# Optimization experiments

Measured on AMD Instinct MI355X. Metric: run time of the kernel, lower is better.

The kernel has to match this reference:

```python
import jax, jax.numpy as jnp
import numpy as np

NUM_HEADS = 16


def rotary_pos_emb(x):
    # x: [b, h, s, d] with interleaved rotary pairs (d even)
    d, s = x.shape[-1], x.shape[-2]
    ts = jnp.arange(0, d, 2, dtype=jnp.float32)
    inv_freqs = 10000.0 ** (-ts / d)                      # [d/2]
    grid = jnp.arange(s, dtype=jnp.float32)[:, None] * inv_freqs[None, :]  # [s, d/2]
    sin = jnp.repeat(jnp.sin(grid), 2, axis=-1)           # [s, d]
    cos = jnp.repeat(jnp.cos(grid), 2, axis=-1)           # [s, d]
    x1, x2 = x[..., ::2], x[..., 1::2]
    xs = jnp.stack([-x2, x1], axis=-1).reshape(x.shape)   # rotate pairs
    return x * cos + xs * sin


def setup_inputs() -> dict:
    key = jax.random.key(0)
    ks = jax.random.split(key, 6)
    b, l, d = 2, 2048, 1024
    x = jax.random.normal(ks[0], (b, l, d), dtype=jnp.float32)
    # additive causal mask: 0 on/below diag, large negative above
    causal = jnp.tril(jnp.ones((l, l), dtype=bool))
    mask = jnp.where(causal, 0.0, -1e9).astype(jnp.float32)[None, None]  # [1,1,l,l]
    s = 0.01  # VarianceScaling(0.01)-ish small init
    Wq = jax.random.normal(ks[1], (d, d), dtype=jnp.float32) * s
    Wk = jax.random.normal(ks[2], (d, d), dtype=jnp.float32) * s
    Wv = jax.random.normal(ks[3], (d, d), dtype=jnp.float32) * s
    Wo = jax.random.normal(ks[4], (d, d), dtype=jnp.float32) * s
    return {"x": x, "mask": mask, "Wq": Wq, "Wk": Wk, "Wv": Wv, "Wo": Wo}


def reference(x, mask, Wq, Wk, Wv, Wo):
    b, l, d = x.shape
    h = NUM_HEADS
    k_sz = d // h
    split = lambda t: t.reshape(b, l, h, k_sz).transpose(0, 2, 1, 3)  # b h l k
    # NOTE: original scales q by 1/sqrt(model_dim) (not key_size), before RoPE
    q = split(x @ Wq / jnp.sqrt(jnp.float32(d)))
    q = rotary_pos_emb(q)
    k = rotary_pos_emb(split(x @ Wk))
    v = split(x @ Wv)
    logits = jnp.einsum('bhik,bhjk->bhij', q, k) + mask   # [b,h,l,l]
    a = jax.nn.softmax(logits, axis=-1)
    y = jnp.einsum('bhij,bhjv->bhiv', a, v)               # [b,h,l,k]
    y = y.transpose(0, 2, 1, 3).reshape(b, l, d)
    return y @ Wo
```

## Files before the change

kernel.cpp:

```cpp
#include <hip/hip_runtime.h>
#include <math.h>

#define L 2048
#define D 1024
#define H 16
#define KS 64
#define BBATCH 2

typedef float f32x4 __attribute__((ext_vector_type(4)));
typedef short s16x8 __attribute__((ext_vector_type(8)));

__device__ __forceinline__ ushort f2bf(float f) {
    union { float f; unsigned u; } v; v.f = f;
    unsigned lsb = (v.u >> 16) & 1u;
    v.u += 0x7fffu + lsb;
    return (ushort)(v.u >> 16);
}

__device__ __forceinline__ unsigned fbits(float f) {
    union { float f; unsigned u; } v; v.f = f; return v.u;
}

__device__ __forceinline__ void gl_lds16(const ushort* g, ushort* l) {
    __builtin_amdgcn_global_load_lds(
        (const __attribute__((address_space(1))) unsigned int*)g,
        (__attribute__((address_space(3))) unsigned int*)l, 16, 0, 0);
}

__global__ __launch_bounds__(256)
void prep(const float* __restrict__ x,
          const float* __restrict__ W0, const float* __restrict__ W1,
          const float* __restrict__ W2, const float* __restrict__ W3,
          ushort* __restrict__ xb, ushort* __restrict__ Wt,
          float2* __restrict__ tab)
{
    __shared__ float T[32][33];
    const int bid = blockIdx.x;
    const int tid = threadIdx.x;
    if (bid < 4096) {
        const int i = bid * 1024 + tid * 4;
        const float4 v = *(const float4*)&x[i];
        ushort4 p = make_ushort4(f2bf(v.x), f2bf(v.y), f2bf(v.z), f2bf(v.w));
        *(ushort4*)&xb[i] = p;
    } else if (bid < 8192) {
        const int t = bid - 4096;
        const int z = t >> 10;
        const float* W = (z == 0) ? W0 : (z == 1) ? W1 : (z == 2) ? W2 : W3;
        ushort* out = Wt + (size_t)z * D * D;
        const int r0 = ((t >> 5) & 31) * 32, c0 = (t & 31) * 32;
        const int tr = tid >> 3, tc = (tid & 7) * 4;
        const float4 v = *(const float4*)&W[(size_t)(r0 + tr) * D + c0 + tc];
        T[tr][tc + 0] = v.x; T[tr][tc + 1] = v.y;
        T[tr][tc + 2] = v.z; T[tr][tc + 3] = v.w;
        __syncthreads();
        ushort4 p = make_ushort4(f2bf(T[tc + 0][tr]), f2bf(T[tc + 1][tr]),
                                 f2bf(T[tc + 2][tr]), f2bf(T[tc + 3][tr]));
        *(ushort4*)&out[(size_t)(c0 + tr) * D + r0 + tc] = p;
    } else {
        const int idx = (bid - 8192) * 256 + tid;
        const int dd2 = idx >> 11, s = idx & 2047;
        const float inv = __expf(-(float)(2 * dd2) * (9.210340371976184f / 64.0f));
        float sn, cs;
        sincosf((float)s * inv, &sn, &cs);
        tab[idx] = make_float2(cs, sn);
    }
}

__global__ __launch_bounds__(256)
void qkv_gemm(const ushort* __restrict__ A, const ushort* __restrict__ B,
              const float2* __restrict__ tab,
              ushort* __restrict__ Qo, ushort* __restrict__ Ko,
              ushort* __restrict__ Vto)
{
    __shared__ __align__(16) ushort smem[18432];
    ushort* As = smem;
    ushort* Bs = smem + 4096;

    const int tid  = threadIdx.x;
    const int wv   = tid >> 6, lane = tid & 63;
    const int i16  = lane & 15, quad = lane >> 4;
    const int wr   = wv >> 1, wc = wv & 1;
    const int m0   = blockIdx.y * 128;
    const int n0   = blockIdx.x * 128;

    f32x4 acc[4][4];
    #pragma unroll
    for (int i = 0; i < 4; ++i)
        #pragma unroll
        for (int j = 0; j < 4; ++j) acc[i][j] = (f32x4){0.f, 0.f, 0.f, 0.f};

    for (int k0 = 0; k0 < D; k0 += 32) {
        __syncthreads();
        {
            int c = wv * 64 + lane;
            gl_lds16(A + (size_t)(m0 + (c >> 2)) * D + k0 + (c & 3) * 8,
                     As + (size_t)(wv * 64) * 8);
            c = 256 + wv * 64 + lane;
            gl_lds16(A + (size_t)(m0 + (c >> 2)) * D + k0 + (c & 3) * 8,
                     As + (size_t)(256 + wv * 64) * 8);
        }
        {
            int c = wv * 64 + lane;
            gl_lds16(B + (size_t)(n0 + (c >> 2)) * D + k0 + (c & 3) * 8,
                     Bs + (size_t)(wv * 64) * 8);
            c = 256 + wv * 64 + lane;
            gl_lds16(B + (size_t)(n0 + (c >> 2)) * D + k0 + (c & 3) * 8,
                     Bs + (size_t)(256 + wv * 64) * 8);
        }
        __syncthreads();
        s16x8 af[4], bf[4];
        #pragma unroll
        for (int mt = 0; mt < 4; ++mt)
            af[mt] = *(const s16x8*)&As[(wr * 64 + mt * 16 + i16) * 32 + quad * 8];
        #pragma unroll
        for (int nt = 0; nt < 4; ++nt)
            bf[nt] = *(const s16x8*)&Bs[(wc * 64 + nt * 16 + i16) * 32 + quad * 8];
        #pragma unroll
        for (int mt = 0; mt < 4; ++mt)
            #pragma unroll
            for (int nt = 0; nt < 4; ++nt)
                acc[mt][nt] = __builtin_amdgcn_mfma_f32_16x16x32_bf16(
                    af[mt], bf[nt], acc[mt][nt], 0, 0, 0);
    }

    if (m0 < 2048) {
        const bool isQ = (m0 < 1024);
        ushort* out = isQ ? Qo : Ko;
        const int mb = isQ ? m0 : (m0 - 1024);
        #pragma unroll
        for (int mt = 0; mt < 4; ++mt)
            #pragma unroll
            for (int nt = 0; nt < 4; ++nt) {
                const int token = n0 + wc * 64 + nt * 16 + i16;
                const int b = token >> 11, s = token & 2047;
                const int dim = mb + wr * 64 + mt * 16 + quad * 4;
                const int hh = dim >> 6, dd = dim & 63;
                ushort4 p;
                #pragma unroll
                for (int pr = 0; pr < 2; ++pr) {
                    float e = acc[mt][nt][2 * pr];
                    float o = acc[mt][nt][2 * pr + 1];
                    if (isQ) { e *= 0.03125f; o *= 0.03125f; }
                    const float2 cssn = tab[(size_t)((dd >> 1) + pr) * 2048 + s];
                    const float ne = e * cssn.x - o * cssn.y;
                    const float no = o * cssn.x + e * cssn.y;
                    if (pr == 0) { p.x = f2bf(ne); p.y = f2bf(no); }
                    else         { p.z = f2bf(ne); p.w = f2bf(no); }
                }
                *(ushort4*)&out[((size_t)(b * H + hh) * L + s) * KS + dd] = p;
            }
    } else {
        __syncthreads();
        ushort* T = smem + wv * 4608;
        const int vbase = (m0 - 2048) + wr * 64;
        const int tbase = n0 + wc * 64;
        #pragma unroll
        for (int mt = 0; mt < 4; ++mt)
            #pragma unroll
            for (int nt = 0; nt < 4; ++nt) {
                const int tl = nt * 16 + i16;
                #pragma unroll
                for (int r = 0; r < 4; ++r)
                    T[(mt * 16 + quad * 4 + r) * 72 + tl] = f2bf(acc[mt][nt][r]);
            }
        __builtin_amdgcn_s_waitcnt(0);
        const int tl0 = (lane & 7) * 8;
        #pragma unroll
        for (int c = 0; c < 8; ++c) {
            const int vl = c * 8 + (lane >> 3);
            const s16x8 val = *(const s16x8*)&T[vl * 72 + tl0];
            const int vdim = vbase + vl;
            const int hh = vdim >> 6, dd = vdim & 63;
            const int token0 = tbase + tl0;
            const int b = token0 >> 11, s0 = token0 & 2047;
            *(s16x8*)&Vto[((size_t)(b * H + hh) * KS + dd) * L + s0] = val;
        }
    }
}

__global__ __launch_bounds__(256)
void oproj_gemm(const ushort* __restrict__ A, const ushort* __restrict__ B,
                float* __restrict__ out)
{
    __shared__ __align__(16) ushort As[128 * 32];
    __shared__ __align__(16) ushort Bs[64 * 32];
    const int tid  = threadIdx.x;
    const int wv   = tid >> 6, lane = tid & 63;
    const int i16  = lane & 15, quad = lane >> 4;
    const int wr   = wv >> 1, wc = wv & 1;
    const int m0   = blockIdx.y * 128;
    const int n0   = blockIdx.x * 64;

    f32x4 acc[4][2];
    #pragma unroll
    for (int i = 0; i < 4; ++i)
        #pragma unroll
        for (int j = 0; j < 2; ++j) acc[i][j] = (f32x4){0.f, 0.f, 0.f, 0.f};

    for (int k0 = 0; k0 < D; k0 += 32) {
        __syncthreads();
        {
            int c = wv * 64 + lane;
            gl_lds16(A + (size_t)(m0 + (c >> 2)) * D + k0 + (c & 3) * 8,
                     As + (size_t)(wv * 64) * 8);
            c = 256 + wv * 64 + lane;
            gl_lds16(A + (size_t)(m0 + (c >> 2)) * D + k0 + (c & 3) * 8,
                     As + (size_t)(256 + wv * 64) * 8);
        }
        {
            int c = wv * 64 + lane;
            gl_lds16(B + (size_t)(n0 + (c >> 2)) * D + k0 + (c & 3) * 8,
                     Bs + (size_t)(wv * 64) * 8);
        }
        __syncthreads();
        s16x8 af[4], bf[2];
        #pragma unroll
        for (int mt = 0; mt < 4; ++mt)
            af[mt] = *(const s16x8*)&As[(wr * 64 + mt * 16 + i16) * 32 + quad * 8];
        #pragma unroll
        for (int nt = 0; nt < 2; ++nt)
            bf[nt] = *(const s16x8*)&Bs[(wc * 32 + nt * 16 + i16) * 32 + quad * 8];
        #pragma unroll
        for (int mt = 0; mt < 4; ++mt)
            #pragma unroll
            for (int nt = 0; nt < 2; ++nt)
                acc[mt][nt] = __builtin_amdgcn_mfma_f32_16x16x32_bf16(
                    af[mt], bf[nt], acc[mt][nt], 0, 0, 0);
    }

    #pragma unroll
    for (int mt = 0; mt < 4; ++mt)
        #pragma unroll
        for (int nt = 0; nt < 2; ++nt) {
            const int od = n0 + wc * 32 + nt * 16 + i16;
            const int tk = m0 + wr * 64 + mt * 16 + quad * 4;
            #pragma unroll
            for (int r = 0; r < 4; ++r)
                out[(size_t)(tk + r) * D + od] = acc[mt][nt][r];
        }
}

__global__ __launch_bounds__(512)
void attn_mfma(const ushort* __restrict__ Q, const ushort* __restrict__ K,
               const ushort* __restrict__ Vt, ushort* __restrict__ Yb)
{
    const int bh   = blockIdx.y;
    const int qa   = blockIdx.x;
    const int qb   = 31 - qa;
    const int tid  = threadIdx.x;
    const int wave = tid >> 6, lane = tid & 63;
    const int half = wave >> 2, wv4 = wave & 3;
    const int i16  = lane & 15, quad = lane >> 4;
    const int qt   = half ? qb : qa;
    const int r0   = qt * 64 + wv4 * 16;
    const int row  = r0 + i16;

    __shared__ ushort Ks[2][64 * 72];
    __shared__ ushort Vs[2][64 * 72];
    __shared__ ushort Ps[8][16 * 72];

    const ushort* Qb = Q  + (size_t)bh * L * KS;
    const ushort* Kb = K  + (size_t)bh * L * KS;
    const ushort* Vb = Vt + (size_t)bh * KS * L;

    const s16x8 qf0 = *(const s16x8*)(Qb + (size_t)row * KS + quad * 8);
    const s16x8 qf1 = *(const s16x8*)(Qb + (size_t)row * KS + 32 + quad * 8);

    const int sr = tid >> 3, sseg = (tid & 7) * 8;
    s16x8 kpre = *(const s16x8*)(Kb + (size_t)sr * KS + sseg);
    s16x8 vpre = *(const s16x8*)(Vb + (size_t)sr * L + sseg);
    *(s16x8*)&Ks[0][sr * 72 + sseg] = kpre;
    *(s16x8*)&Vs[0][sr * 72 + sseg] = vpre;
    __syncthreads();

    f32x4 O0 = {0.f,0.f,0.f,0.f}, O1 = O0, O2 = O0, O3 = O0;
    float psum = 0.0f;

    for (int jt = 0; jt <= qb; ++jt) {
        const int cur = jt & 1;
        const bool has_next = (jt < qb);

        if (has_next) {
            const int j0n = (jt + 1) * 64;
            kpre = *(const s16x8*)(Kb + (size_t)(j0n + sr) * KS + sseg);
            vpre = *(const s16x8*)(Vb + (size_t)sr * L + j0n + sseg);
        }

        if (jt <= qt) {
            const int j0 = jt * 64;
            const ushort* Ksb = &Ks[cur][0];
            const ushort* Vsb = &Vs[cur][0];
            f32x4 st[4];
            #pragma unroll
            for (int nt = 0; nt < 4; ++nt) {
                const s16x8 kf0 = *(const s16x8*)&Ksb[(nt * 16 + i16) * 72 + quad * 8];
                const s16x8 kf1 = *(const s16x8*)&Ksb[(nt * 16 + i16) * 72 + 32 + quad * 8];
                f32x4 c = {0.f,0.f,0.f,0.f};
                c = __builtin_amdgcn_mfma_f32_16x16x32_bf16(kf0, qf0, c, 0, 0, 0);
                c = __builtin_amdgcn_mfma_f32_16x16x32_bf16(kf1, qf1, c, 0, 0, 0);
                st[nt] = c;
            }
            if (jt == qt) {
                #pragma unroll
                for (int nt = 0; nt < 4; ++nt)
                    #pragma unroll
                    for (int rg = 0; rg < 4; ++rg) {
                        const int j = j0 + nt * 16 + quad * 4 + rg;
                        if (j > row) st[nt][rg] = -1e30f;
                    }
            }
            float pv[4][4];
            #pragma unroll
            for (int nt = 0; nt < 4; ++nt)
                #pragma unroll
                for (int rg = 0; rg < 4; ++rg) {
                    pv[nt][rg] = __expf(st[nt][rg]);
                    psum += pv[nt][rg];
                }
            ushort* P2 = &Ps[wave][0];
            #pragma unroll
            for (int nt = 0; nt < 4; ++nt) {
                uint2 pk;
                pk.x = __builtin_amdgcn_perm(fbits(pv[nt][1]), fbits(pv[nt][0]), 0x07060302u);
                pk.y = __builtin_amdgcn_perm(fbits(pv[nt][3]), fbits(pv[nt][2]), 0x07060302u);
                *(uint2*)(P2 + i16 * 72 + nt * 16 + quad * 4) = pk;
            }
            const s16x8 pf0 = *(const s16x8*)(P2 + i16 * 72 + quad * 8);
            const s16x8 pf1 = *(const s16x8*)(P2 + i16 * 72 + 32 + quad * 8);
            s16x8 v0, v1;
            v0 = *(const s16x8*)&Vsb[(0 * 16 + i16) * 72 + quad * 8];
            v1 = *(const s16x8*)&Vsb[(0 * 16 + i16) * 72 + 32 + quad * 8];
            O0 = __builtin_amdgcn_mfma_f32_16x16x32_bf16(v0, pf0, O0, 0, 0, 0);
            O0 = __builtin_amdgcn_mfma_f32_16x16x32_bf16(v1, pf1, O0, 0, 0, 0);
            v0 = *(const s16x8*)&Vsb[(1 * 16 + i16) * 72 + quad * 8];
            v1 = *(const s16x8*)&Vsb[(1 * 16 + i16) * 72 + 32 + quad * 8];
            O1 = __builtin_amdgcn_mfma_f32_16x16x32_bf16(v0, pf0, O1, 0, 0, 0);
            O1 = __builtin_amdgcn_mfma_f32_16x16x32_bf16(v1, pf1, O1, 0, 0, 0);
            v0 = *(const s16x8*)&Vsb[(2 * 16 + i16) * 72 + quad * 8];
            v1 = *(const s16x8*)&Vsb[(2 * 16 + i16) * 72 + 32 + quad * 8];
            O2 = __builtin_amdgcn_mfma_f32_16x16x32_bf16(v0, pf0, O2, 0, 0, 0);
            O2 = __builtin_amdgcn_mfma_f32_16x16x32_bf16(v1, pf1, O2, 0, 0, 0);
            v0 = *(const s16x8*)&Vsb[(3 * 16 + i16) * 72 + quad * 8];
            v1 = *(const s16x8*)&Vsb[(3 * 16 + i16) * 72 + 32 + quad * 8];
            O3 = __builtin_amdgcn_mfma_f32_16x16x32_bf16(v0, pf0, O3, 0, 0, 0);
            O3 = __builtin_amdgcn_mfma_f32_16x16x32_bf16(v1, pf1, O3, 0, 0, 0);
        }

        if (has_next) {
            *(s16x8*)&Ks[cur ^ 1][sr * 72 + sseg] = kpre;
            *(s16x8*)&Vs[cur ^ 1][sr * 72 + sseg] = vpre;
            __syncthreads();
        }
    }

    psum += __shfl_xor(psum, 16);
    psum += __shfl_xor(psum, 32);
    const float inv_l = __builtin_amdgcn_rcpf(psum);
    const int b = bh >> 4, hh = bh & 15;
    ushort* Yp = Yb + ((size_t)(b * L + row)) * D + hh * KS + quad * 4;
    f32x4 r;
    r = O0 * inv_l; *(ushort4*)(Yp +  0) = make_ushort4(f2bf(r[0]),f2bf(r[1]),f2bf(r[2]),f2bf(r[3]));
    r = O1 * inv_l; *(ushort4*)(Yp + 16) = make_ushort4(f2bf(r[0]),f2bf(r[1]),f2bf(r[2]),f2bf(r[3]));
    r = O2 * inv_l; *(ushort4*)(Yp + 32) = make_ushort4(f2bf(r[0]),f2bf(r[1]),f2bf(r[2]),f2bf(r[3]));
    r = O3 * inv_l; *(ushort4*)(Yp + 48) = make_ushort4(f2bf(r[0]),f2bf(r[1]),f2bf(r[2]),f2bf(r[3]));
}

extern "C" void kernel_launch(void* const* d_in, const int* in_sizes, int n_in,
                              void* d_out, int out_size, void* d_ws, size_t ws_size,
                              hipStream_t stream)
{
    const float* x  = (const float*)d_in[0];
    const float* Wq = (const float*)d_in[2];
    const float* Wk = (const float*)d_in[3];
    const float* Wv = (const float*)d_in[4];
    const float* Wo = (const float*)d_in[5];

    const size_t NTOK = (size_t)BBATCH * L;
    const size_t SZ   = NTOK * D;
    ushort* xb  = (ushort*)d_ws;
    ushort* Wt  = xb + SZ;
    ushort* Qb  = Wt + 4 * (size_t)D * D;
    ushort* Kb  = Qb + SZ;
    ushort* Vtb = Kb + SZ;
    ushort* Yb  = Vtb + SZ;
    float2* tab = (float2*)Yb;

    prep<<<dim3(8448), dim3(256), 0, stream>>>(x, Wq, Wk, Wv, Wo, xb, Wt, tab);

    qkv_gemm<<<dim3(32, 24), dim3(256), 0, stream>>>(Wt, xb, tab, Qb, Kb, Vtb);

    attn_mfma<<<dim3(16, 32), dim3(512), 0, stream>>>(Qb, Kb, Vtb, Yb);

    oproj_gemm<<<dim3(16, 32), dim3(256), 0, stream>>>(Yb, Wt + 3 * (size_t)D * D,
                                                       (float*)d_out);
}
```

Measured before the change: 200.9 us.

## Double-buffer LDS tiles in QKV and output-projection GEMMs

Both GEMM kernels now use two LDS tile buffers. The next K-slice is issued with global_load_lds into the idle buffer while MFMAs run on the current one, and only one barrier per iteration remains instead of two. The aim is to hide global-load latency behind matrix math. The cost is twice the LDS footprint in oproj (qkv reuses its existing shared array), which can lower occupancy. The overlap also depends on the end-of-loop barrier waiting for the async loads to finish.

```diff
diff --git a/kernel.cpp b/kernel.cpp
--- a/kernel.cpp
+++ b/kernel.cpp
@@ -73,9 +73,6 @@
               ushort* __restrict__ Vto)
 {
     __shared__ __align__(16) ushort smem[18432];
-    ushort* As = smem;
-    ushort* Bs = smem + 4096;
-
     const int tid  = threadIdx.x;
     const int wv   = tid >> 6, lane = tid & 63;
     const int i16  = lane & 15, quad = lane >> 4;
@@ -83,31 +80,37 @@
     const int m0   = blockIdx.y * 128;
     const int n0   = blockIdx.x * 128;
 
+    const int cA0 = wv * 64 + lane, cA1 = 256 + wv * 64 + lane;
+
     f32x4 acc[4][4];
     #pragma unroll
     for (int i = 0; i < 4; ++i)
         #pragma unroll
         for (int j = 0; j < 4; ++j) acc[i][j] = (f32x4){0.f, 0.f, 0.f, 0.f};
 
-    for (int k0 = 0; k0 < D; k0 += 32) {
-        __syncthreads();
-        {
-            int c = wv * 64 + lane;
-            gl_lds16(A + (size_t)(m0 + (c >> 2)) * D + k0 + (c & 3) * 8,
-                     As + (size_t)(wv * 64) * 8);
-            c = 256 + wv * 64 + lane;
-            gl_lds16(A + (size_t)(m0 + (c >> 2)) * D + k0 + (c & 3) * 8,
-                     As + (size_t)(256 + wv * 64) * 8);
-        }
-        {
-            int c = wv * 64 + lane;
-            gl_lds16(B + (size_t)(n0 + (c >> 2)) * D + k0 + (c & 3) * 8,
-                     Bs + (size_t)(wv * 64) * 8);
-            c = 256 + wv * 64 + lane;
-            gl_lds16(B + (size_t)(n0 + (c >> 2)) * D + k0 + (c & 3) * 8,
-                     Bs + (size_t)(256 + wv * 64) * 8);
-        }
-        __syncthreads();
+    {
+        ushort* As = smem;
+        ushort* Bs = smem + 4096;
+        gl_lds16(A + (size_t)(m0 + (cA0 >> 2)) * D + (cA0 & 3) * 8, As + (size_t)(wv * 64) * 8);
+        gl_lds16(A + (size_t)(m0 + (cA1 >> 2)) * D + (cA1 & 3) * 8, As + (size_t)(256 + wv * 64) * 8);
+        gl_lds16(B + (size_t)(n0 + (cA0 >> 2)) * D + (cA0 & 3) * 8, Bs + (size_t)(wv * 64) * 8);
+        gl_lds16(B + (size_t)(n0 + (cA1 >> 2)) * D + (cA1 & 3) * 8, Bs + (size_t)(256 + wv * 64) * 8);
+    }
+    __syncthreads();
+
+    for (int it = 0; it < 32; ++it) {
+        const int cur = it & 1;
+        if (it + 1 < 32) {
+            const int kn = (it + 1) * 32;
+            ushort* As = smem + (cur ^ 1) * 8192;
+            ushort* Bs = As + 4096;
+            gl_lds16(A + (size_t)(m0 + (cA0 >> 2)) * D + kn + (cA0 & 3) * 8, As + (size_t)(wv * 64) * 8);
+            gl_lds16(A + (size_t)(m0 + (cA1 >> 2)) * D + kn + (cA1 & 3) * 8, As + (size_t)(256 + wv * 64) * 8);
+            gl_lds16(B + (size_t)(n0 + (cA0 >> 2)) * D + kn + (cA0 & 3) * 8, Bs + (size_t)(wv * 64) * 8);
+            gl_lds16(B + (size_t)(n0 + (cA1 >> 2)) * D + kn + (cA1 & 3) * 8, Bs + (size_t)(256 + wv * 64) * 8);
+        }
+        const ushort* As = smem + cur * 8192;
+        const ushort* Bs = As + 4096;
         s16x8 af[4], bf[4];
         #pragma unroll
         for (int mt = 0; mt < 4; ++mt)
@@ -121,6 +124,7 @@
             for (int nt = 0; nt < 4; ++nt)
                 acc[mt][nt] = __builtin_amdgcn_mfma_f32_16x16x32_bf16(
                     af[mt], bf[nt], acc[mt][nt], 0, 0, 0);
+        __syncthreads();
     }
 
     if (m0 < 2048) {
@@ -150,7 +154,6 @@
                 *(ushort4*)&out[((size_t)(b * H + hh) * L + s) * KS + dd] = p;
             }
     } else {
-        __syncthreads();
         ushort* T = smem + wv * 4608;
         const int vbase = (m0 - 2048) + wr * 64;
         const int tbase = n0 + wc * 64;
@@ -182,8 +185,7 @@
 void oproj_gemm(const ushort* __restrict__ A, const ushort* __restrict__ B,
                 float* __restrict__ out)
 {
-    __shared__ __align__(16) ushort As[128 * 32];
-    __shared__ __align__(16) ushort Bs[64 * 32];
+    __shared__ __align__(16) ushort smem[12288];
     const int tid  = threadIdx.x;
     const int wv   = tid >> 6, lane = tid & 63;
     const int i16  = lane & 15, quad = lane >> 4;
@@ -191,28 +193,35 @@
     const int m0   = blockIdx.y * 128;
     const int n0   = blockIdx.x * 64;
 
+    const int cA0 = wv * 64 + lane, cA1 = 256 + wv * 64 + lane;
+
     f32x4 acc[4][2];
     #pragma unroll
     for (int i = 0; i < 4; ++i)
         #pragma unroll
         for (int j = 0; j < 2; ++j) acc[i][j] = (f32x4){0.f, 0.f, 0.f, 0.f};
 
-    for (int k0 = 0; k0 < D; k0 += 32) {
-        __syncthreads();
-        {
-            int c = wv * 64 + lane;
-            gl_lds16(A + (size_t)(m0 + (c >> 2)) * D + k0 + (c & 3) * 8,
-                     As + (size_t)(wv * 64) * 8);
-            c = 256 + wv * 64 + lane;
-            gl_lds16(A + (size_t)(m0 + (c >> 2)) * D + k0 + (c & 3) * 8,
-                     As + (size_t)(256 + wv * 64) * 8);
-        }
-        {
-            int c = wv * 64 + lane;
-            gl_lds16(B + (size_t)(n0 + (c >> 2)) * D + k0 + (c & 3) * 8,
-                     Bs + (size_t)(wv * 64) * 8);
-        }
-        __syncthreads();
+    {
+        ushort* As = smem;
+        ushort* Bs = smem + 4096;
+        gl_lds16(A + (size_t)(m0 + (cA0 >> 2)) * D + (cA0 & 3) * 8, As + (size_t)(wv * 64) * 8);
+        gl_lds16(A + (size_t)(m0 + (cA1 >> 2)) * D + (cA1 & 3) * 8, As + (size_t)(256 + wv * 64) * 8);
+        gl_lds16(B + (size_t)(n0 + (cA0 >> 2)) * D + (cA0 & 3) * 8, Bs + (size_t)(wv * 64) * 8);
+    }
+    __syncthreads();
+
+    for (int it = 0; it < 32; ++it) {
+        const int cur = it & 1;
+        if (it + 1 < 32) {
+            const int kn = (it + 1) * 32;
+            ushort* As = smem + (cur ^ 1) * 6144;
+            ushort* Bs = As + 4096;
+            gl_lds16(A + (size_t)(m0 + (cA0 >> 2)) * D + kn + (cA0 & 3) * 8, As + (size_t)(wv * 64) * 8);
+            gl_lds16(A + (size_t)(m0 + (cA1 >> 2)) * D + kn + (cA1 & 3) * 8, As + (size_t)(256 + wv * 64) * 8);
+            gl_lds16(B + (size_t)(n0 + (cA0 >> 2)) * D + kn + (cA0 & 3) * 8, Bs + (size_t)(wv * 64) * 8);
+        }
+        const ushort* As = smem + cur * 6144;
+        const ushort* Bs = As + 4096;
         s16x8 af[4], bf[2];
         #pragma unroll
         for (int mt = 0; mt < 4; ++mt)
@@ -226,6 +235,7 @@
             for (int nt = 0; nt < 2; ++nt)
                 acc[mt][nt] = __builtin_amdgcn_mfma_f32_16x16x32_bf16(
                     af[mt], bf[nt], acc[mt][nt], 0, 0, 0);
+        __syncthreads();
     }
 
     #pragma unroll
```

Result: faster. 194.2 us (-3.4%).
